# Optimization experiments

Hardware: AMD Instinct MI355X
Metric: run time of the kernel (lower is better)

## Reference

```python
import jax, jax.numpy as jnp
import numpy as np
from functools import partial

B, C, FD, H, W = 8, 256, 128, 64, 64
POSC = 34  # 32 learned pos channels + 2 raw meshgrid channels


def create_meshgrid(h, w):
    # kornia-style normalized grid in [-1, 1], returned as [1, 2, h, w] (x, y)
    xs = jnp.linspace(-1.0, 1.0, w, dtype=jnp.float32)
    ys = jnp.linspace(-1.0, 1.0, h, dtype=jnp.float32)
    gy, gx = jnp.meshgrid(ys, xs, indexing='ij')
    return jnp.stack([gx, gy], axis=0)[None]  # [1,2,h,w]


def conv1x1(x, w, b):
    return jnp.einsum('bchw,oc->bohw', x, w) + b[None, :, None, None]


def pos_gen(feat, pg_w1, pg_b1, pg_w2, pg_b2):
    # PosGen type=2 with detach: two 1x1 'mul' layers (conv + ReLU, no norm)
    b, c, h, w = feat.shape
    feat = jax.lax.stop_gradient(feat)
    pos = jnp.broadcast_to(create_meshgrid(h, w), (b, 2, h, w))
    inp = jnp.concatenate([pos + 1.0, feat], axis=1)           # [b, feat_dim+2, h, w]
    h1 = jax.nn.relu(conv1x1(inp, pg_w1, pg_b1))               # [b, feat_dim, h, w]
    h2 = jax.nn.relu(conv1x1(h1, pg_w2, pg_b2))                # [b, 32, h, w]
    return jnp.concatenate([h2, pos], axis=1)                  # [b, 34, h, w]


def fuser(x, feat, w1, b1, w2, b2):
    # fuser_1D: concat along channels, 1x1 -> hidden (ReLU) -> 1x1 -> 256
    z = jnp.concatenate([x, feat], axis=1)
    z = jax.nn.relu(conv1x1(z, w1, b1))
    return conv1x1(z, w2, b2)


def conv_y(y, dw_w, dw_b, pw_w, pw_b):
    # BasicDWLayer: depthwise 3x3 + pointwise 1x1, no norm, no activation
    z = jax.lax.conv_general_dilated(
        y, dw_w, window_strides=(1, 1), padding='SAME',
        feature_group_count=y.shape[1],
        dimension_numbers=('NCHW', 'OIHW', 'NCHW')) + dw_b[None, :, None, None]
    return conv1x1(z, pw_w, pw_b)


def matching_forward(x, y, feat1, feat2,
                     pg_w1, pg_b1, pg_w2, pg_b2,
                     fus_w1, fus_b1, fus_w2, fus_b2,
                     dw_w, dw_b, pw_w, pw_b,
                     dustbin_vec, dustbin_pos):
    b, c, hx, wx = x.shape
    hy, wy = y.shape[2], y.shape[3]

    posf = pos_gen(feat2, pg_w1, pg_b1, pg_w2, pg_b2)          # [b, 34, hy, wy]
    c_pose = posf.shape[1]
    pos = posf.reshape(b, 1, c_pose, hy * wy).swapaxes(-1, -2)  # [b,1,Nk,34]

    xf = fuser(x, feat1, fus_w1, fus_b1, fus_w2, fus_b2)
    yf = fuser(y, feat2, fus_w1, fus_b1, fus_w2, fus_b2)
    yf = conv_y(yf, dw_w, dw_b, pw_w, pw_b)
    d = yf.shape[1]

    q = xf.reshape(b, 1, d, hx * wx).swapaxes(-1, -2)           # [b,1,Nq,256]
    k = yf.reshape(b, 1, d, hy * wy).swapaxes(-1, -2)           # [b,1,Nk,256]

    # dustbin token augmentation
    k = jnp.concatenate([k, jnp.broadcast_to(dustbin_vec, (b, 1, 1, d))], axis=-2)
    pos = jnp.concatenate([pos, jnp.broadcast_to(dustbin_pos, (b, 1, 1, c_pose))], axis=-2)

    # single-head cross-attention: values are the positional channels
    scores = jnp.einsum('bhqc,bhkc->bhqk', q, k) / jnp.sqrt(jnp.float32(d))
    attn = jax.nn.softmax(scores, axis=-1)
    out = jnp.einsum('bhqk,bhkd->bhqd', attn, pos)              # [b,1,Nq,34]
    return out.swapaxes(-1, -2).reshape(b, c_pose, hx, wx)


def setup_inputs() -> dict:
    key = jax.random.key(0)
    ks = jax.random.split(key, 20)
    s = 0.05
    return {
        'x': jax.random.normal(ks[0], (B, C, H, W), jnp.float32),
        'y': jax.random.normal(ks[1], (B, C, H, W), jnp.float32),
        'feat1': jax.random.normal(ks[2], (B, FD, H, W), jnp.float32),
        'feat2': jax.random.normal(ks[3], (B, FD, H, W), jnp.float32),
        # PosGen type-2 mapping: (feat_dim+2)->feat_dim, feat_dim->(hidden-2=32)
        'pg_w1': jax.random.normal(ks[4], (FD, FD + 2), jnp.float32) * s,
        'pg_b1': jnp.zeros((FD,), jnp.float32),
        'pg_w2': jax.random.normal(ks[5], (32, FD), jnp.float32) * s,
        'pg_b2': jnp.zeros((32,), jnp.float32),
        # fuser_1D: (256+128)->256 hidden, hidden->256
        'fus_w1': jax.random.normal(ks[6], (256, C + FD), jnp.float32) * s,
        'fus_b1': jnp.zeros((256,), jnp.float32),
        'fus_w2': jax.random.normal(ks[7], (C, 256), jnp.float32) * s,
        'fus_b2': jnp.zeros((C,), jnp.float32),
        # conv_y: depthwise 3x3 + pointwise 1x1
        'dw_w': jax.random.normal(ks[8], (C, 1, 3, 3), jnp.float32) * s,
        'dw_b': jnp.zeros((C,), jnp.float32),
        'pw_w': jax.random.normal(ks[9], (C, C), jnp.float32) * s,
        'pw_b': jnp.zeros((C,), jnp.float32),
        'dustbin_vec': jax.random.uniform(ks[10], (1, 1, 1, C), jnp.float32) / 10.0,
        'dustbin_pos': jnp.zeros((1, 1, 1, POSC), jnp.float32) - 10.0,
    }


def reference(x, y, feat1, feat2,
              pg_w1, pg_b1, pg_w2, pg_b2,
              fus_w1, fus_b1, fus_w2, fus_b2,
              dw_w, dw_b, pw_w, pw_b,
              dustbin_vec, dustbin_pos):
    return matching_forward(x, y, feat1, feat2,
                            pg_w1, pg_b1, pg_w2, pg_b2,
                            fus_w1, fus_b1, fus_w2, fus_b2,
                            dw_w, dw_b, pw_w, pw_b,
                            dustbin_vec, dustbin_pos)
```

## Files before the change

kernel.cpp:

```cpp
#include <hip/hip_runtime.h>
#include <hip/hip_bf16.h>

typedef __hip_bfloat16 bf16;
typedef unsigned short ushort_t;
typedef __bf16 bf16x8 __attribute__((ext_vector_type(8)));
typedef float  f32x4  __attribute__((ext_vector_type(4)));

#define HW    4096
#define NB    8
#define KSTR  4160
#define NTOK  32768
#define PROWS 64
#define QSCALE 0.0901684400557f

__device__ __forceinline__ float lde(const void* p, size_t i, int f32f) {
    return f32f ? ((const float*)p)[i] : (float)((const bf16*)p)[i];
}
__device__ __forceinline__ ushort_t f2bu(float f){ union { __bf16 b; ushort_t u; } cv; cv.b = (__bf16)f; return cv.u; }

__device__ __forceinline__ void async_cp16(const void* g, void* l) {
    __builtin_amdgcn_global_load_lds(
        (const __attribute__((address_space(1))) unsigned int*)g,
        (__attribute__((address_space(3))) unsigned int*)l, 16, 0, 0);
}

__global__ void detect_kernel(const ushort_t* xb, int* flag)
{
    __shared__ int cnt;
    const int t = threadIdx.x;
    if (t == 0) cnt = 0;
    __syncthreads();
    ushort_t h = xb[2*t];
    int e = (h >> 7) & 0xFF;
    if (e >= 133) atomicAdd(&cnt, 1);
    __syncthreads();
    if (t == 0) *flag = (cnt > 8) ? 1 : 0;
}

struct WsPtrs {
    bf16 *fw1t, *fw2t, *pwt, *pgw1t, *pgw2t, *dwt, *pos;
    float *posw, *fb1, *fb2, *pwb, *pgb1, *pgb2, *dwb;
};

__global__ __launch_bounds__(256) void prep_kernel(
    const void* fus_w1, const void* fus_w2, const void* pw_w,
    const void* pg_w1, const void* pg_w2, const void* dw_w,
    const void* fus_b1, const void* fus_b2, const void* pw_b,
    const void* pg_b1, const void* pg_b2, const void* dw_b,
    const void* dpos, WsPtrs W, const int* flag)
{
    const int f = *flag;
    const long n_w1 = 98304, n_w2 = 65536, n_pw = 65536, n_g1 = 16384, n_g2 = 4096;
    const long n_posw = 256, n_dwt = 2304;
    const long n_b = 256, n_gb1 = 128, n_gb2 = 32;
    const long n_mesh = 65536;
    const long n_pad  = 8L*14*KSTR;
    const long n_dust = 272;
    const long n_zt   = 8L*34*63;
    const long total = n_w1+n_w2+n_pw+n_g1+n_g2+n_posw+n_dwt
                     + 3*n_b + n_gb1 + n_gb2 + n_b + n_mesh + n_pad + n_dust + n_zt;

    for (long i = blockIdx.x*256L + threadIdx.x; i < total; i += gridDim.x*256L) {
        long j = i;
        if (j < n_w1) { W.fw1t[j] = __float2bfloat16(lde(fus_w1, j, f)); continue; } j -= n_w1;
        if (j < n_w2) { W.fw2t[j] = __float2bfloat16(lde(fus_w2, j, f)); continue; } j -= n_w2;
        if (j < n_pw) { W.pwt[j]  = __float2bfloat16(lde(pw_w,  j, f)); continue; } j -= n_pw;
        if (j < n_g1) { W.pgw1t[j] = __float2bfloat16(lde(pg_w1, (j>>7)*130 + 2 + (j&127), f)); continue; } j -= n_g1;
        if (j < n_g2) { W.pgw2t[j] = __float2bfloat16(lde(pg_w2, j, f)); continue; } j -= n_g2;
        if (j < n_posw) { W.posw[j] = lde(pg_w1, (j>>1)*130 + (j&1), f); continue; } j -= n_posw;
        if (j < n_dwt) { W.dwt[j] = __float2bfloat16(lde(dw_w, (j&255)*9 + (j>>8), f)); continue; } j -= n_dwt;
        if (j < n_b)   { W.fb1[j] = lde(fus_b1, j, f); continue; } j -= n_b;
        if (j < n_b)   { W.fb2[j] = lde(fus_b2, j, f); continue; } j -= n_b;
        if (j < n_b)   { W.pwb[j] = lde(pw_b, j, f); continue; } j -= n_b;
        if (j < n_gb1) { W.pgb1[j] = lde(pg_b1, j, f); continue; } j -= n_gb1;
        if (j < n_gb2) { W.pgb2[j] = lde(pg_b2, j, f); continue; } j -= n_gb2;
        if (j < n_b)   { W.dwb[j] = lde(dw_b, j, f); continue; } j -= n_b;
        if (j < n_mesh) {
            long b = j >> 13; int rr = (int)((j>>12)&1); int tok = (int)(j & 4095);
            float v = rr ? (-1.f + 2.f*(float)((tok>>6)&63)/63.f)
                         : (-1.f + 2.f*(float)(tok&63)/63.f);
            W.pos[((size_t)b*PROWS + 32 + rr)*KSTR + tok] = __float2bfloat16(v);
            continue;
        } j -= n_mesh;
        if (j < n_pad) {
            long b = j / (14L*KSTR); long rem = j % (14L*KSTR);
            int row = 34 + (int)(rem / KSTR); int tok = (int)(rem % KSTR);
            W.pos[((size_t)b*PROWS + row)*KSTR + tok] = __float2bfloat16(row == 34 ? 1.f : 0.f);
            continue;
        } j -= n_pad;
        if (j < n_dust) {
            long b = j / 34; int ch = (int)(j % 34);
            W.pos[((size_t)b*PROWS + ch)*KSTR + 4096] = __float2bfloat16(lde(dpos, ch, f));
            continue;
        } j -= n_dust;
        { long b = j / (34*63); long rem = j % (34*63);
          int ch = (int)(rem / 63); int cc = (int)(rem % 63);
          W.pos[((size_t)b*PROWS + ch)*KSTR + 4097 + cc] = __float2bfloat16(0.f); }
    }
}

__global__ __launch_bounds__(256) void transpose_kernel(
    const void* main_src, const void* feat_src, bf16* __restrict__ dst, const int* flag)
{
    __shared__ float Tt[64*65];
    const int t = threadIdx.x;
    const int p0 = blockIdx.x * 64;
    const int cht = blockIdx.y;
    const int b = blockIdx.z;
    const int f = *flag;

    const void* src; int ch0, srcC, dc0;
    if (cht < 4) { src = main_src; ch0 = cht*64; srcC = 256; dc0 = ch0; }
    else         { src = feat_src; ch0 = (cht-4)*64; srcC = 128; dc0 = 256 + (cht-4)*64; }

    const int p = t & 63, cq = t >> 6;
    #pragma unroll
    for (int e = 0; e < 16; ++e) {
        int c = e*4 + cq;
        Tt[p*65 + c] = lde(src, ((size_t)b*srcC + ch0 + c)*HW + p0 + p, f);
    }
    __syncthreads();
    const int pr = t >> 2, cs = (t & 3) * 16;
    union { uint4 u4[2]; ushort_t us[16]; } pk;
    #pragma unroll
    for (int u = 0; u < 16; ++u) pk.us[u] = f2bu(Tt[pr*65 + cs + u]);
    ushort_t* op = (ushort_t*)dst + ((size_t)b*HW + p0 + pr)*384 + dc0 + cs;
    *(uint4*)op = pk.u4[0];
    *((uint4*)op + 1) = pk.u4[1];
}

template<int MT, bool RELU, bool POSEPI, int OMODE>
__global__ __launch_bounds__(256) void gemm_mfma(
    const bf16* __restrict__ A, int sa,
    const bf16* __restrict__ Bw, int ldb,
    const float* __restrict__ bias, const float* __restrict__ posw,
    bf16* __restrict__ out, int sm, int K, float oscale)
{
    const int t = threadIdx.x;
    const int w = t >> 6, lane = t & 63;
    const int n = lane & 15, quad = lane >> 4;
    const int p0 = blockIdx.x * 128;
    const int m0 = blockIdx.y * (MT*16);
    const int rowbase = p0 + w*32;

    f32x4 acc[2][MT];
    #pragma unroll
    for (int pt = 0; pt < 2; ++pt)
        #pragma unroll
        for (int mt = 0; mt < MT; ++mt) acc[pt][mt] = (f32x4){0.f,0.f,0.f,0.f};

    for (int k0 = 0; k0 < K; k0 += 32) {
        bf16x8 ap[2];
        #pragma unroll
        for (int pt = 0; pt < 2; ++pt)
            ap[pt] = *(const bf16x8*)&A[(size_t)(rowbase + pt*16 + n)*sa + k0 + quad*8];
        #pragma unroll
        for (int mt = 0; mt < MT; ++mt) {
            bf16x8 bw = *(const bf16x8*)&Bw[(size_t)(m0 + mt*16 + n)*ldb + k0 + quad*8];
            acc[0][mt] = __builtin_amdgcn_mfma_f32_16x16x32_bf16(ap[0], bw, acc[0][mt], 0, 0, 0);
            acc[1][mt] = __builtin_amdgcn_mfma_f32_16x16x32_bf16(ap[1], bw, acc[1][mt], 0, 0, 0);
        }
    }

    #pragma unroll
    for (int mt = 0; mt < MT; ++mt) {
        const int m = m0 + mt*16 + n;
        const float bi = bias[m];
        float w0 = 0.f, w1 = 0.f;
        if (POSEPI) { w0 = posw[m*2]; w1 = posw[m*2 + 1]; }
        #pragma unroll
        for (int pt = 0; pt < 2; ++pt) {
            const int tokb = rowbase + pt*16 + quad*4;
            if (OMODE == 1) {
                union { uint2 u2; ushort_t us[4]; } pk;
                #pragma unroll
                for (int r = 0; r < 4; ++r) {
                    float v = acc[pt][mt][r] + bi;
                    if (RELU) v = fmaxf(v, 0.f);
                    pk.us[r] = f2bu(v * oscale);
                }
                size_t oi = ((size_t)(tokb >> 12)*PROWS + m)*KSTR + (tokb & 4095);
                *(uint2*)((ushort_t*)out + oi) = pk.u2;
            } else {
                #pragma unroll
                for (int r = 0; r < 4; ++r) {
                    int tok = tokb + r;
                    float v = acc[pt][mt][r] + bi;
                    if (POSEPI) {
                        float gx1 = 2.f * (float)(tok & 63) / 63.f;
                        float gy1 = 2.f * (float)((tok >> 6) & 63) / 63.f;
                        v += w0*gx1 + w1*gy1;
                    }
                    if (RELU) v = fmaxf(v, 0.f);
                    v *= oscale;
                    size_t row = (OMODE == 2) ? (size_t)tok + 64*(size_t)(tok >> 12) : (size_t)tok;
                    out[row*sm + m] = __float2bfloat16(v);
                }
            }
        }
    }
}

__global__ __launch_bounds__(256) void dw_kernel(
    const bf16* __restrict__ in, const bf16* __restrict__ dwt,
    const float* __restrict__ dwb, bf16* __restrict__ out)
{
    const int t = threadIdx.x;
    const int tok = blockIdx.x*8 + (t >> 5);
    const int c8 = (t & 31) * 8;
    const int b = tok >> 12, p = tok & 4095;
    const int i = p >> 6, j = p & 63;

    float acc[8];
    #pragma unroll
    for (int u = 0; u < 8; ++u) acc[u] = dwb[c8 + u];

    #pragma unroll
    for (int di = 0; di < 3; ++di) {
        int ii = i + di - 1;
        if (ii < 0 || ii >= 64) continue;
        #pragma unroll
        for (int dj = 0; dj < 3; ++dj) {
            int jj = j + dj - 1;
            if (jj < 0 || jj >= 64) continue;
            int tok2 = (b << 12) + ii*64 + jj;
            bf16x8 xv = *(const bf16x8*)&in[(size_t)tok2*256 + c8];
            bf16x8 wv = *(const bf16x8*)&dwt[(di*3 + dj)*256 + c8];
            #pragma unroll
            for (int u = 0; u < 8; ++u) acc[u] += (float)xv[u] * (float)wv[u];
        }
    }
    union { uint4 u4; ushort_t us[8]; } pk;
    #pragma unroll
    for (int u = 0; u < 8; ++u) pk.us[u] = f2bu(acc[u]);
    *(uint4*)((ushort_t*)out + (size_t)tok*256 + c8) = pk.u4;
}

__global__ __launch_bounds__(256) void fill_late_kernel(
    const void* dvec, bf16* __restrict__ k_t, const int* flag)
{
    const int b = blockIdx.x, t = threadIdx.x;
    k_t[((size_t)b*KSTR + 4096)*256 + t] = __float2bfloat16(lde(dvec, t, *flag));
}

__global__ __launch_bounds__(256, 2) void attn_kernel(
    const bf16* __restrict__ q_t, const bf16* __restrict__ k_t,
    const bf16* __restrict__ pos, void* outv, const int* flag)
{
    __shared__ __align__(16) __bf16 Ks[2048*8];
    __shared__ __align__(16) __bf16 posb[512*8];
    __shared__ __align__(16) __bf16 Pb[64*72];

    const int t = threadIdx.x;
    const int w = t >> 6, lane = t & 63;
    const int n = lane & 15, quad = lane >> 4;
    const int bid = blockIdx.x;
    const int b = bid & 7;
    const int qt = bid >> 3;

    bf16x8 aq[8];
    {
        size_t qrow = (size_t)b*HW + qt*64 + w*16 + n;
        #pragma unroll
        for (int c = 0; c < 8; ++c)
            aq[c] = *(const bf16x8*)&q_t[qrow*256 + c*32 + quad*8];
    }

    f32x4 pacc[3];
    #pragma unroll
    for (int ct = 0; ct < 3; ++ct) pacc[ct] = (f32x4){0.f,0.f,0.f,0.f};

    const ushort_t* ksrc0 = (const ushort_t*)k_t + (size_t)b*KSTR*256;
    const ushort_t* psrc0 = (const ushort_t*)pos + (size_t)b*PROWS*KSTR;
    const int xw = n & 7;

    for (int kt = 0; kt < 65; ++kt) {
        const int kbase = kt*64;

        __syncthreads();
        #pragma unroll
        for (int e = 0; e < 8; ++e) {
            int slot = w*512 + e*64 + lane;
            int tok = slot >> 5;
            int ch = ((slot & 31) ^ (tok & 7)) * 8;
            async_cp16(&ksrc0[(size_t)(kbase + tok)*256 + ch], &Ks[(size_t)slot*8]);
        }
        #pragma unroll
        for (int e = 0; e < 2; ++e) {
            int slot = w*128 + e*64 + lane;
            int row = slot >> 3;
            int ch = ((slot & 7) ^ (row & 7)) * 8;
            async_cp16(&psrc0[(size_t)row*KSTR + kbase + ch], &posb[(size_t)slot*8]);
        }
        __syncthreads();

        f32x4 sacc[4];
        #pragma unroll
        for (int nt = 0; nt < 4; ++nt) sacc[nt] = (f32x4){0.f,0.f,0.f,0.f};
        #pragma unroll
        for (int c = 0; c < 8; ++c) {
            #pragma unroll
            for (int nt = 0; nt < 4; ++nt) {
                bf16x8 bk = *(const bf16x8*)&Ks[(size_t)((nt*16 + n)*32 + ((c*4 + quad) ^ xw))*8];
                sacc[nt] = __builtin_amdgcn_mfma_f32_16x16x32_bf16(aq[c], bk, sacc[nt], 0, 0, 0);
            }
        }

        #pragma unroll
        for (int nt = 0; nt < 4; ++nt) {
            const bool ok = (kbase + nt*16 + n) <= 4096;
            #pragma unroll
            for (int r = 0; r < 4; ++r) {
                float pv = ok ? __builtin_amdgcn_exp2f(sacc[nt][r]) : 0.f;
                Pb[(w*16 + quad*4 + r)*72 + nt*16 + n] = (__bf16)pv;
            }
        }

        #pragma unroll
        for (int c = 0; c < 2; ++c) {
            bf16x8 aP = *(const bf16x8*)&Pb[(w*16 + n)*72 + c*32 + quad*8];
            #pragma unroll
            for (int ct = 0; ct < 3; ++ct) {
                bf16x8 bp = *(const bf16x8*)&posb[(size_t)((ct*16 + n)*8 + ((c*4 + quad) ^ xw))*8];
                pacc[ct] = __builtin_amdgcn_mfma_f32_16x16x32_bf16(aP, bp, pacc[ct], 0, 0, 0);
            }
        }
    }

    const int f32o = *flag;
    float linv[4];
    #pragma unroll
    for (int r = 0; r < 4; ++r)
        linv[r] = 1.f / __shfl(pacc[2][r], (lane & 48) | 2, 64);
    #pragma unroll
    for (int ct = 0; ct < 3; ++ct) {
        int ch = ct*16 + n;
        if (ch >= 34) continue;
        #pragma unroll
        for (int r = 0; r < 4; ++r) {
            float v = pacc[ct][r] * linv[r];
            size_t oi = ((size_t)b*34 + ch)*HW + qt*64 + w*16 + quad*4 + r;
            if (f32o) ((float*)outv)[oi] = v;
            else      ((bf16*)outv)[oi]  = __float2bfloat16(v);
        }
    }
}

extern "C" void kernel_launch(void* const* d_in, const int* in_sizes, int n_in,
                              void* d_out, int out_size, void* d_ws, size_t ws_size,
                              hipStream_t stream)
{
    const void* x      = d_in[0];
    const void* y      = d_in[1];
    const void* feat1  = d_in[2];
    const void* feat2  = d_in[3];
    const void* pg_w1  = d_in[4];
    const void* pg_b1  = d_in[5];
    const void* pg_w2  = d_in[6];
    const void* pg_b2  = d_in[7];
    const void* fus_w1 = d_in[8];
    const void* fus_b1 = d_in[9];
    const void* fus_w2 = d_in[10];
    const void* fus_b2 = d_in[11];
    const void* dw_w   = d_in[12];
    const void* dw_b   = d_in[13];
    const void* pw_w   = d_in[14];
    const void* pw_b   = d_in[15];
    const void* dvec   = d_in[16];
    const void* dpos   = d_in[17];

    char* wsb = (char*)d_ws;
    int*  flag = (int*)wsb;
    size_t off = 16;
    bf16* R1   = (bf16*)(wsb + off); off += (size_t)NTOK*384*2;
    bf16* bufH = (bf16*)(wsb + off); off += (size_t)NTOK*256*2;
    bf16* q_t  = (bf16*)(wsb + off); off += (size_t)NTOK*256*2;
    bf16* pos  = (bf16*)(wsb + off); off += (size_t)NB*PROWS*KSTR*2;
    WsPtrs W;
    W.fw1t  = (bf16*)(wsb + off); off += 98304*2;
    W.fw2t  = (bf16*)(wsb + off); off += 65536*2;
    W.pwt   = (bf16*)(wsb + off); off += 65536*2;
    W.pgw1t = (bf16*)(wsb + off); off += 16384*2;
    W.pgw2t = (bf16*)(wsb + off); off += 4096*2;
    W.dwt   = (bf16*)(wsb + off); off += 2304*2;
    W.pos   = pos;
    W.posw  = (float*)(wsb + off); off += 256*4;
    W.fb1   = (float*)(wsb + off); off += 256*4;
    W.fb2   = (float*)(wsb + off); off += 256*4;
    W.pwb   = (float*)(wsb + off); off += 256*4;
    W.pgb1  = (float*)(wsb + off); off += 128*4;
    W.pgb2  = (float*)(wsb + off); off += 32*4;
    W.dwb   = (float*)(wsb + off); off += 256*4;

    bf16* in_xy = R1;
    bf16* yf    = R1;
    bf16* k_t   = R1;

    dim3 b256(256);

    detect_kernel<<<1, 256, 0, stream>>>((const ushort_t*)x, flag);
    prep_kernel<<<1024, b256, 0, stream>>>(fus_w1, fus_w2, pw_w, pg_w1, pg_w2, dw_w,
                                           fus_b1, fus_b2, pw_b, pg_b1, pg_b2, dw_b,
                                           dpos, W, flag);
    transpose_kernel<<<dim3(64,6,NB), b256, 0, stream>>>(x, feat1, in_xy, flag);
    gemm_mfma<8, true, false, 0><<<dim3(256,2), b256, 0, stream>>>(
        in_xy, 384, W.fw1t, 384, W.fb1, nullptr, bufH, 256, 384, 1.f);
    gemm_mfma<8, false, false, 0><<<dim3(256,2), b256, 0, stream>>>(
        bufH, 256, W.fw2t, 256, W.fb2, nullptr, q_t, 256, 256, QSCALE);
    transpose_kernel<<<dim3(64,6,NB), b256, 0, stream>>>(y, feat2, in_xy, flag);
    gemm_mfma<8, true, true, 0><<<dim3(256,1), b256, 0, stream>>>(
        in_xy + 256, 384, W.pgw1t, 128, W.pgb1, W.posw, bufH, 128, 128, 1.f);
    gemm_mfma<2, true, false, 1><<<dim3(256,1), b256, 0, stream>>>(
        bufH, 128, W.pgw2t, 128, W.pgb2, nullptr, pos, 0, 128, 1.f);
    gemm_mfma<8, true, false, 0><<<dim3(256,2), b256, 0, stream>>>(
        in_xy, 384, W.fw1t, 384, W.fb1, nullptr, bufH, 256, 384, 1.f);
    gemm_mfma<8, false, false, 0><<<dim3(256,2), b256, 0, stream>>>(
        bufH, 256, W.fw2t, 256, W.fb2, nullptr, yf, 256, 256, 1.f);
    dw_kernel<<<dim3(4096), b256, 0, stream>>>(yf, W.dwt, W.dwb, bufH);
    fill_late_kernel<<<dim3(NB), b256, 0, stream>>>(dvec, k_t, flag);
    gemm_mfma<8, false, false, 2><<<dim3(256,2), b256, 0, stream>>>(
        bufH, 256, W.pwt, 256, W.pwb, nullptr, k_t, 256, 256, 1.f);
    attn_kernel<<<dim3(512), b256, 0, stream>>>(q_t, k_t, pos, d_out, flag);
}
```

Before: 500.3 us.

## Triple-buffer attention key/pos tiles with async prefetch and halve tile size

Reworks the attention kernel's K/pos streaming loop. Key tiles shrink from 64 to 32 tokens and are kept in three LDS buffers. The next tile is prefetched with async global-to-LDS copies while the current one is computed, using a vmcnt wait and a single barrier per iteration instead of two blocking barriers. The goal is to hide global load latency behind MFMA work. In exchange, LDS use grows, there are twice as many loop iterations with fewer MFMAs each, and the pos buffer loses its XOR swizzle, which may cause bank conflicts.

```diff
diff --git a/kernel.cpp b/kernel.cpp
--- a/kernel.cpp
+++ b/kernel.cpp
@@ -12,6 +12,9 @@
 #define NTOK  32768
 #define PROWS 64
 #define QSCALE 0.0901684400557f
+
+#define KT3   32
+#define NKT3  130
 
 __device__ __forceinline__ float lde(const void* p, size_t i, int f32f) {
     return f32f ? ((const float*)p)[i] : (float)((const bf16*)p)[i];
@@ -247,9 +250,9 @@
     const bf16* __restrict__ q_t, const bf16* __restrict__ k_t,
     const bf16* __restrict__ pos, void* outv, const int* flag)
 {
-    __shared__ __align__(16) __bf16 Ks[2048*8];
-    __shared__ __align__(16) __bf16 posb[512*8];
-    __shared__ __align__(16) __bf16 Pb[64*72];
+    __shared__ __align__(16) __bf16 Ks[3*1024*8];
+    __shared__ __align__(16) __bf16 posb[3*256*8];
+    __shared__ __align__(16) __bf16 Pb[64*40];
 
     const int t = threadIdx.x;
     const int w = t >> 6, lane = t & 63;
@@ -274,58 +277,70 @@
     const ushort_t* psrc0 = (const ushort_t*)pos + (size_t)b*PROWS*KSTR;
     const int xw = n & 7;
 
-    for (int kt = 0; kt < 65; ++kt) {
-        const int kbase = kt*64;
-
-        __syncthreads();
-        #pragma unroll
-        for (int e = 0; e < 8; ++e) {
-            int slot = w*512 + e*64 + lane;
+    auto STAGE = [&](int kt2, int bufn) {
+        const int kb = kt2 * KT3;
+        __bf16* kd = &Ks[(size_t)bufn*8192];
+        #pragma unroll
+        for (int e = 0; e < 4; ++e) {
+            int slot = w*256 + e*64 + lane;
             int tok = slot >> 5;
             int ch = ((slot & 31) ^ (tok & 7)) * 8;
-            async_cp16(&ksrc0[(size_t)(kbase + tok)*256 + ch], &Ks[(size_t)slot*8]);
-        }
-        #pragma unroll
-        for (int e = 0; e < 2; ++e) {
-            int slot = w*128 + e*64 + lane;
-            int row = slot >> 3;
-            int ch = ((slot & 7) ^ (row & 7)) * 8;
-            async_cp16(&psrc0[(size_t)row*KSTR + kbase + ch], &posb[(size_t)slot*8]);
-        }
-        __syncthreads();
-
-        f32x4 sacc[4];
-        #pragma unroll
-        for (int nt = 0; nt < 4; ++nt) sacc[nt] = (f32x4){0.f,0.f,0.f,0.f};
+            async_cp16(&ksrc0[(size_t)(kb + tok)*256 + ch], &kd[(size_t)slot*8]);
+        }
+        {
+            int slot = w*64 + lane;
+            int row = slot >> 2;
+            int ch = (slot & 3) * 8;
+            async_cp16(&psrc0[(size_t)row*KSTR + kb + ch], &posb[(size_t)(bufn*256 + slot)*8]);
+        }
+    };
+
+    STAGE(0, 0);
+    int bc = 0, bn = 1;
+    for (int kt = 0; kt < NKT3; ++kt) {
+        STAGE(kt + 1 < NKT3 ? kt + 1 : 0, bn);
+        asm volatile("s_waitcnt vmcnt(5)" ::: "memory");
+        __builtin_amdgcn_s_barrier();
+        asm volatile("" ::: "memory");
+
+        const int kbase = kt * KT3;
+        const __bf16* kb_ = &Ks[(size_t)bc*8192];
+        const __bf16* pb_ = &posb[(size_t)bc*2048];
+
+        f32x4 sacc[2];
+        sacc[0] = (f32x4){0.f,0.f,0.f,0.f};
+        sacc[1] = (f32x4){0.f,0.f,0.f,0.f};
         #pragma unroll
         for (int c = 0; c < 8; ++c) {
             #pragma unroll
-            for (int nt = 0; nt < 4; ++nt) {
-                bf16x8 bk = *(const bf16x8*)&Ks[(size_t)((nt*16 + n)*32 + ((c*4 + quad) ^ xw))*8];
+            for (int nt = 0; nt < 2; ++nt) {
+                bf16x8 bk = *(const bf16x8*)&kb_[(size_t)((nt*16 + n)*32 + ((c*4 + quad) ^ xw))*8];
                 sacc[nt] = __builtin_amdgcn_mfma_f32_16x16x32_bf16(aq[c], bk, sacc[nt], 0, 0, 0);
             }
         }
 
         #pragma unroll
-        for (int nt = 0; nt < 4; ++nt) {
+        for (int nt = 0; nt < 2; ++nt) {
             const bool ok = (kbase + nt*16 + n) <= 4096;
             #pragma unroll
             for (int r = 0; r < 4; ++r) {
                 float pv = ok ? __builtin_amdgcn_exp2f(sacc[nt][r]) : 0.f;
-                Pb[(w*16 + quad*4 + r)*72 + nt*16 + n] = (__bf16)pv;
+                Pb[(w*16 + quad*4 + r)*40 + nt*16 + n] = (__bf16)pv;
             }
         }
 
-        #pragma unroll
-        for (int c = 0; c < 2; ++c) {
-            bf16x8 aP = *(const bf16x8*)&Pb[(w*16 + n)*72 + c*32 + quad*8];
+        {
+            bf16x8 aP = *(const bf16x8*)&Pb[(w*16 + n)*40 + quad*8];
             #pragma unroll
             for (int ct = 0; ct < 3; ++ct) {
-                bf16x8 bp = *(const bf16x8*)&posb[(size_t)((ct*16 + n)*8 + ((c*4 + quad) ^ xw))*8];
+                bf16x8 bp = *(const bf16x8*)&pb_[(size_t)((ct*16 + n)*4 + quad)*8];
                 pacc[ct] = __builtin_amdgcn_mfma_f32_16x16x32_bf16(aP, bp, pacc[ct], 0, 0, 0);
             }
         }
-    }
+
+        int b3 = 3 - bc - bn; bc = bn; bn = b3;
+    }
+    asm volatile("s_waitcnt vmcnt(0)" ::: "memory");
 
     const int f32o = *flag;
     float linv[4];
```

After: 502.6 us. About the same (+0.5%).

## Double-buffer attention K/pos tiles and widen blocks to 128 queries

Applied to the files above, without the earlier changes.

The attention kernel now runs 512-thread blocks that each handle 128 queries. Each wave owns 4 query fragments and one 16-key slice, so every staged K tile serves twice as many queries. K and pos tiles are double-buffered in LDS, and the next tile is loaded asynchronously while the current one is computed, using explicit waitcnt and barrier calls in place of two __syncthreads per step. LDS use grows to roughly 98KB per block, which limits residency to one block per CU. There are also fewer blocks in total (256), so latency hiding relies on the prefetch.

```diff
diff --git a/kernel.cpp b/kernel.cpp
--- a/kernel.cpp
+++ b/kernel.cpp
@@ -243,27 +243,29 @@
     k_t[((size_t)b*KSTR + 4096)*256 + t] = __float2bfloat16(lde(dvec, t, *flag));
 }
 
-__global__ __launch_bounds__(256, 2) void attn_kernel(
+__global__ __launch_bounds__(512, 2) void attn_kernel(
     const bf16* __restrict__ q_t, const bf16* __restrict__ k_t,
     const bf16* __restrict__ pos, void* outv, const int* flag)
 {
-    __shared__ __align__(16) __bf16 Ks[2048*8];
-    __shared__ __align__(16) __bf16 posb[512*8];
-    __shared__ __align__(16) __bf16 Pb[64*72];
+    __shared__ __align__(16) __bf16 Ks[2*2048*8];
+    __shared__ __align__(16) __bf16 posb[2*512*8];
+    __shared__ __align__(16) __bf16 Pb[2*64*72];
 
     const int t = threadIdx.x;
     const int w = t >> 6, lane = t & 63;
     const int n = lane & 15, quad = lane >> 4;
+    const int qg = w >> 2, ks = w & 3;
     const int bid = blockIdx.x;
     const int b = bid & 7;
     const int qt = bid >> 3;
 
-    bf16x8 aq[8];
-    {
-        size_t qrow = (size_t)b*HW + qt*64 + w*16 + n;
+    bf16x8 aq[4][8];
+    #pragma unroll
+    for (int f = 0; f < 4; ++f) {
+        size_t qrow = (size_t)b*HW + qt*128 + qg*64 + f*16 + n;
         #pragma unroll
         for (int c = 0; c < 8; ++c)
-            aq[c] = *(const bf16x8*)&q_t[qrow*256 + c*32 + quad*8];
+            aq[f][c] = *(const bf16x8*)&q_t[qrow*256 + c*32 + quad*8];
     }
 
     f32x4 pacc[3];
@@ -274,58 +276,71 @@
     const ushort_t* psrc0 = (const ushort_t*)pos + (size_t)b*PROWS*KSTR;
     const int xw = n & 7;
 
-    for (int kt = 0; kt < 65; ++kt) {
-        const int kbase = kt*64;
-
-        __syncthreads();
-        #pragma unroll
-        for (int e = 0; e < 8; ++e) {
-            int slot = w*512 + e*64 + lane;
+    auto STAGE = [&](int kt2, int bufn) {
+        const int kb = kt2 * 64;
+        __bf16* kd = &Ks[(size_t)bufn*16384];
+        #pragma unroll
+        for (int e = 0; e < 4; ++e) {
+            int slot = w*256 + e*64 + lane;
             int tok = slot >> 5;
             int ch = ((slot & 31) ^ (tok & 7)) * 8;
-            async_cp16(&ksrc0[(size_t)(kbase + tok)*256 + ch], &Ks[(size_t)slot*8]);
-        }
-        #pragma unroll
-        for (int e = 0; e < 2; ++e) {
-            int slot = w*128 + e*64 + lane;
+            async_cp16(&ksrc0[(size_t)(kb + tok)*256 + ch], &kd[(size_t)slot*8]);
+        }
+        {
+            int slot = w*64 + lane;
             int row = slot >> 3;
             int ch = ((slot & 7) ^ (row & 7)) * 8;
-            async_cp16(&psrc0[(size_t)row*KSTR + kbase + ch], &posb[(size_t)slot*8]);
-        }
-        __syncthreads();
+            async_cp16(&psrc0[(size_t)row*KSTR + kb + ch], &posb[(size_t)(bufn*512 + slot)*8]);
+        }
+    };
+
+    STAGE(0, 0);
+    for (int kt = 0; kt < 65; ++kt) {
+        const int cur = kt & 1;
+        asm volatile("s_waitcnt vmcnt(0)" ::: "memory");
+        __builtin_amdgcn_s_barrier();
+        asm volatile("" ::: "memory");
+        if (kt + 1 < 65) STAGE(kt + 1, cur ^ 1);
+
+        const __bf16* kb_ = &Ks[(size_t)cur*16384];
+        const __bf16* pb_ = &posb[(size_t)cur*4096];
+        __bf16* Pq = &Pb[(size_t)qg*(64*72)];
 
         f32x4 sacc[4];
         #pragma unroll
-        for (int nt = 0; nt < 4; ++nt) sacc[nt] = (f32x4){0.f,0.f,0.f,0.f};
+        for (int f = 0; f < 4; ++f) sacc[f] = (f32x4){0.f,0.f,0.f,0.f};
         #pragma unroll
         for (int c = 0; c < 8; ++c) {
+            bf16x8 bk = *(const bf16x8*)&kb_[(size_t)((ks*16 + n)*32 + ((c*4 + quad) ^ xw))*8];
             #pragma unroll
-            for (int nt = 0; nt < 4; ++nt) {
-                bf16x8 bk = *(const bf16x8*)&Ks[(size_t)((nt*16 + n)*32 + ((c*4 + quad) ^ xw))*8];
-                sacc[nt] = __builtin_amdgcn_mfma_f32_16x16x32_bf16(aq[c], bk, sacc[nt], 0, 0, 0);
-            }
-        }
-
-        #pragma unroll
-        for (int nt = 0; nt < 4; ++nt) {
-            const bool ok = (kbase + nt*16 + n) <= 4096;
+            for (int f = 0; f < 4; ++f)
+                sacc[f] = __builtin_amdgcn_mfma_f32_16x16x32_bf16(aq[f][c], bk, sacc[f], 0, 0, 0);
+        }
+
+        const bool ok = (kt*64 + ks*16 + n) <= 4096;
+        #pragma unroll
+        for (int f = 0; f < 4; ++f)
             #pragma unroll
             for (int r = 0; r < 4; ++r) {
-                float pv = ok ? __builtin_amdgcn_exp2f(sacc[nt][r]) : 0.f;
-                Pb[(w*16 + quad*4 + r)*72 + nt*16 + n] = (__bf16)pv;
+                float pv = ok ? __builtin_amdgcn_exp2f(sacc[f][r]) : 0.f;
+                Pq[(f*16 + quad*4 + r)*72 + ks*16 + n] = (__bf16)pv;
             }
-        }
+
+        asm volatile("s_waitcnt lgkmcnt(0)" ::: "memory");
+        __builtin_amdgcn_s_barrier();
+        asm volatile("" ::: "memory");
 
         #pragma unroll
         for (int c = 0; c < 2; ++c) {
-            bf16x8 aP = *(const bf16x8*)&Pb[(w*16 + n)*72 + c*32 + quad*8];
+            bf16x8 aP = *(const bf16x8*)&Pq[(size_t)((ks*16 + n)*72 + c*32 + quad*8)];
             #pragma unroll
             for (int ct = 0; ct < 3; ++ct) {
-                bf16x8 bp = *(const bf16x8*)&posb[(size_t)((ct*16 + n)*8 + ((c*4 + quad) ^ xw))*8];
+                bf16x8 bp = *(const bf16x8*)&pb_[(size_t)((ct*16 + n)*8 + ((c*4 + quad) ^ xw))*8];
                 pacc[ct] = __builtin_amdgcn_mfma_f32_16x16x32_bf16(aP, bp, pacc[ct], 0, 0, 0);
             }
         }
     }
+    asm volatile("s_waitcnt vmcnt(0)" ::: "memory");
 
     const int f32o = *flag;
     float linv[4];
@@ -339,7 +354,7 @@
         #pragma unroll
         for (int r = 0; r < 4; ++r) {
             float v = pacc[ct][r] * linv[r];
-            size_t oi = ((size_t)b*34 + ch)*HW + qt*64 + w*16 + quad*4 + r;
+            size_t oi = ((size_t)b*34 + ch)*HW + qt*128 + qg*64 + ks*16 + quad*4 + r;
             if (f32o) ((float*)outv)[oi] = v;
             else      ((bf16*)outv)[oi]  = __float2bfloat16(v);
         }
@@ -420,5 +435,5 @@
     fill_late_kernel<<<dim3(NB), b256, 0, stream>>>(dvec, k_t, flag);
     gemm_mfma<8, false, false, 2><<<dim3(256,2), b256, 0, stream>>>(
         bufH, 256, W.pwt, 256, W.pwb, nullptr, k_t, 256, 256, 1.f);
-    attn_kernel<<<dim3(512), b256, 0, stream>>>(q_t, k_t, pos, d_out, flag);
-}
+    attn_kernel<<<dim3(256), dim3(512), 0, stream>>>(q_t, k_t, pos, d_out, flag);
+}
```

After: 499.0 us. About the same (-0.3%).
